# Optimization experiments

Hardware: AMD Instinct MI355X
Metric: run time of the kernel (lower is better)

The kernel has to match this reference:

```python
import jax, jax.numpy as jnp
import numpy as np

B, S, D, H = 4, 2048, 1024, 16
HD = D // H  # head_dim = 64


def setup_inputs() -> dict:
    key = jax.random.key(0)
    ks = jax.random.split(key, 9)
    sd = 1.0 / np.sqrt(D)
    x = jax.random.normal(ks[0], (B, S, D), dtype=jnp.float32)
    Wq = jax.random.normal(ks[1], (D, D), dtype=jnp.float32) * sd
    Wk = jax.random.normal(ks[2], (D, D), dtype=jnp.float32) * sd
    Wv = jax.random.normal(ks[3], (D, D), dtype=jnp.float32) * sd
    Wo = jax.random.normal(ks[4], (D, D), dtype=jnp.float32) * sd
    bq = jax.random.normal(ks[5], (D,), dtype=jnp.float32) * sd
    bk = jax.random.normal(ks[6], (D,), dtype=jnp.float32) * sd
    bv = jax.random.normal(ks[7], (D,), dtype=jnp.float32) * sd
    bo = jax.random.normal(ks[8], (D,), dtype=jnp.float32) * sd
    return {"x": x, "Wq": Wq, "bq": bq, "Wk": Wk, "bk": bk,
            "Wv": Wv, "bv": bv, "Wo": Wo, "bo": bo}


def reference(x, Wq, bq, Wk, bk, Wv, bv, Wo, bo):
    b, s, d = x.shape
    scale = jnp.float32(np.sqrt(HD))
    # projections, split into heads: (b, h, s, hd)
    def heads(y):
        return y.reshape(b, s, H, HD).transpose(0, 2, 1, 3)
    Q = heads(x @ Wq + bq)
    K = heads(x @ Wk + bk)
    V = heads(x @ Wv + bv)
    # (b, h, s, s) scores with causal mask
    scores = jnp.einsum('bhqd,bhkd->bhqk', Q, K) / scale
    causal = jnp.tril(jnp.ones((s, s), dtype=bool))
    scores = jnp.where(causal[None, None], scores, jnp.float32(-jnp.inf))
    probs = jax.nn.softmax(scores, axis=-1)
    out = jnp.einsum('bhqk,bhkd->bhqd', probs, V)
    out = out.transpose(0, 2, 1, 3).reshape(b, s, d)
    return out @ Wo + bo
```

## Files before the change

kernel.cpp:

```cpp
#include <hip/hip_runtime.h>
#include <hip/hip_bf16.h>
#include <cstdint>

typedef __bf16 bf16x8 __attribute__((ext_vector_type(8)));
typedef float f32x4 __attribute__((ext_vector_type(4)));
typedef float f32x16 __attribute__((ext_vector_type(16)));
typedef unsigned short u16t;

__device__ __forceinline__ u16t f2bf(float f) {
    uint32_t u = __builtin_bit_cast(uint32_t, f);
    u += 0x7FFF + ((u >> 16) & 1);
    return (u16t)(u >> 16);
}

constexpr int Bb = 4, Ss = 2048, Dd = 1024, Hh = 16;
constexpr int Mrows = Bb * Ss;
constexpr float NEG = -1e30f;
constexpr float QSCALE = 0.125f * 1.44269504088896340736f;

__global__ __launch_bounds__(256) void cvt_bf16(const float* __restrict__ in,
                                                u16t* __restrict__ out, int n) {
    int i = (blockIdx.x * 256 + threadIdx.x) * 4;
    if (i >= n) return;
    float4 v = *(const float4*)(in + i);
    u16t o[4] = {f2bf(v.x), f2bf(v.y), f2bf(v.z), f2bf(v.w)};
    *(ushort4*)(out + i) = *(ushort4*)o;
}

__global__ __launch_bounds__(256) void transpose_cvt4(const float* __restrict__ W0,
                                                      const float* __restrict__ W1,
                                                      const float* __restrict__ W2,
                                                      const float* __restrict__ W3,
                                                      u16t* __restrict__ Tqkv,
                                                      u16t* __restrict__ To) {
    __shared__ float tile[64][65];
    int z = blockIdx.z;
    const float* W = z == 0 ? W0 : z == 1 ? W1 : z == 2 ? W2 : W3;
    u16t* WT = z < 3 ? Tqkv + (size_t)z * Dd * Dd : To;
    int n0 = blockIdx.x * 64, k0 = blockIdx.y * 64;
    int c = threadIdx.x & 63, r0 = (threadIdx.x >> 6) * 16;
    for (int i = 0; i < 16; i++)
        tile[c][r0 + i] = W[(size_t)(k0 + r0 + i) * Dd + n0 + c];
    __syncthreads();
    for (int i = 0; i < 16; i++)
        WT[(size_t)(n0 + r0 + i) * Dd + k0 + c] = f2bf(tile[r0 + i][c]);
}

__global__ __launch_bounds__(256) void gemm_qkv(const u16t* __restrict__ A,
                                                const u16t* __restrict__ BT,
                                                const float* __restrict__ bq,
                                                const float* __restrict__ bk,
                                                const float* __restrict__ bvv,
                                                u16t* __restrict__ Qh,
                                                u16t* __restrict__ Kh,
                                                u16t* __restrict__ Vt) {
    __shared__ __align__(16) u16t Asm[128 * 32];
    __shared__ __align__(16) u16t Bsm[128 * 32];
    int tid = threadIdx.x, lane = tid & 63, w = tid >> 6;
    int wm = w >> 1, wn = w & 1;
    int ln = lane & 15, g = lane >> 4;
    int bid = blockIdx.x;
    int wg = (bid & 7) * 192 + (bid >> 3);
    int n0 = (wg % 24) * 128, m0 = (wg / 24) * 128;

    f32x4 acc[4][4] = {};

    int sr = w * 32 + (lane >> 2);
    int sc = (((lane & 3) ^ (sr & 3)) * 8);
    const u16t* Ag0 = A + (size_t)(m0 + sr) * Dd + sc;
    const u16t* Ag1 = A + (size_t)(m0 + sr + 16) * Dd + sc;
    const u16t* Bg0 = BT + (size_t)(n0 + sr) * Dd + sc;
    const u16t* Bg1 = BT + (size_t)(n0 + sr + 16) * Dd + sc;
    u16t* As0 = &Asm[(w * 32) * 32];
    u16t* As1 = &Asm[(w * 32 + 16) * 32];
    u16t* Bs0 = &Bsm[(w * 32) * 32];
    u16t* Bs1 = &Bsm[(w * 32 + 16) * 32];

    for (int k0 = 0; k0 < Dd; k0 += 32) {
        __syncthreads();
        __builtin_amdgcn_global_load_lds(Ag0 + k0, As0, 16, 0, 0);
        __builtin_amdgcn_global_load_lds(Ag1 + k0, As1, 16, 0, 0);
        __builtin_amdgcn_global_load_lds(Bg0 + k0, Bs0, 16, 0, 0);
        __builtin_amdgcn_global_load_lds(Bg1 + k0, Bs1, 16, 0, 0);
        __syncthreads();
        bf16x8 af[4], bf[4];
        #pragma unroll
        for (int i = 0; i < 4; i++) {
            int row = wm * 64 + i * 16 + ln;
            af[i] = *(const bf16x8*)&Asm[row * 32 + ((g ^ (row & 3)) * 8)];
        }
        #pragma unroll
        for (int j = 0; j < 4; j++) {
            int row = wn * 64 + j * 16 + ln;
            bf[j] = *(const bf16x8*)&Bsm[row * 32 + ((g ^ (row & 3)) * 8)];
        }
        #pragma unroll
        for (int i = 0; i < 4; i++)
            #pragma unroll
            for (int j = 0; j < 4; j++)
                acc[i][j] = __builtin_amdgcn_mfma_f32_16x16x32_bf16(af[i], bf[j], acc[i][j], 0, 0, 0);
    }

    #pragma unroll
    for (int i = 0; i < 4; i++) {
        #pragma unroll
        for (int j = 0; j < 4; j++) {
            int col = n0 + wn * 64 + j * 16 + ln;
            int seg = col >> 10, c1k = col & 1023;
            float bias = seg == 0 ? bq[c1k] : seg == 1 ? bk[c1k] : bvv[c1k];
            int rowb = m0 + wm * 64 + i * 16 + g * 4;
            int b = rowb >> 11, s = rowb & 2047, h = c1k >> 6, hd = c1k & 63;
            if (seg == 0) {
                for (int r = 0; r < 4; r++) {
                    float v = (acc[i][j][r] + bias) * QSCALE;
                    Qh[((size_t)(b * Hh + h) * Ss + s + r) * 64 + hd] = f2bf(v);
                }
            } else if (seg == 1) {
                for (int r = 0; r < 4; r++)
                    Kh[((size_t)(b * Hh + h) * Ss + s + r) * 64 + hd] = f2bf(acc[i][j][r] + bias);
            } else {
                u16t pk4[4];
                for (int r = 0; r < 4; r++) pk4[r] = f2bf(acc[i][j][r] + bias);
                *(ushort4*)(Vt + ((size_t)((b * Hh + h) * 64 + hd) << 11) + s) = *(ushort4*)pk4;
            }
        }
    }
}

__global__ __launch_bounds__(256) void gemm_o(const u16t* __restrict__ A,
                                              const u16t* __restrict__ BT,
                                              const float* __restrict__ bias,
                                              float* __restrict__ outF) {
    __shared__ __align__(16) u16t Asm[128 * 32];
    __shared__ __align__(16) u16t Bsm[128 * 32];
    int tid = threadIdx.x, lane = tid & 63, w = tid >> 6;
    int wm = w >> 1, wn = w & 1;
    int ln = lane & 15, g = lane >> 4;
    int bid = blockIdx.x;
    int wg = (bid & 7) * 64 + (bid >> 3);
    int n0 = (wg & 7) * 128, m0 = (wg >> 3) * 128;

    f32x4 acc[4][4] = {};

    int sr = w * 32 + (lane >> 2);
    int sc = (((lane & 3) ^ (sr & 3)) * 8);
    const u16t* Ag0 = A + (size_t)(m0 + sr) * Dd + sc;
    const u16t* Ag1 = A + (size_t)(m0 + sr + 16) * Dd + sc;
    const u16t* Bg0 = BT + (size_t)(n0 + sr) * Dd + sc;
    const u16t* Bg1 = BT + (size_t)(n0 + sr + 16) * Dd + sc;
    u16t* As0 = &Asm[(w * 32) * 32];
    u16t* As1 = &Asm[(w * 32 + 16) * 32];
    u16t* Bs0 = &Bsm[(w * 32) * 32];
    u16t* Bs1 = &Bsm[(w * 32 + 16) * 32];

    for (int k0 = 0; k0 < Dd; k0 += 32) {
        __syncthreads();
        __builtin_amdgcn_global_load_lds(Ag0 + k0, As0, 16, 0, 0);
        __builtin_amdgcn_global_load_lds(Ag1 + k0, As1, 16, 0, 0);
        __builtin_amdgcn_global_load_lds(Bg0 + k0, Bs0, 16, 0, 0);
        __builtin_amdgcn_global_load_lds(Bg1 + k0, Bs1, 16, 0, 0);
        __syncthreads();
        bf16x8 af[4], bf[4];
        #pragma unroll
        for (int i = 0; i < 4; i++) {
            int row = wm * 64 + i * 16 + ln;
            af[i] = *(const bf16x8*)&Asm[row * 32 + ((g ^ (row & 3)) * 8)];
        }
        #pragma unroll
        for (int j = 0; j < 4; j++) {
            int row = wn * 64 + j * 16 + ln;
            bf[j] = *(const bf16x8*)&Bsm[row * 32 + ((g ^ (row & 3)) * 8)];
        }
        #pragma unroll
        for (int i = 0; i < 4; i++)
            #pragma unroll
            for (int j = 0; j < 4; j++)
                acc[i][j] = __builtin_amdgcn_mfma_f32_16x16x32_bf16(af[i], bf[j], acc[i][j], 0, 0, 0);
    }

    #pragma unroll
    for (int i = 0; i < 4; i++) {
        #pragma unroll
        for (int j = 0; j < 4; j++) {
            int col = n0 + wn * 64 + j * 16 + ln;
            float bv = bias[col];
            int rowb = m0 + wm * 64 + i * 16 + g * 4;
            for (int r = 0; r < 4; r++)
                outF[(size_t)(rowb + r) * Dd + col] = acc[i][j][r] + bv;
        }
    }
}

__global__ __launch_bounds__(256) void attn(const u16t* __restrict__ Qh,
                                            const u16t* __restrict__ Kh,
                                            const u16t* __restrict__ Vt,
                                            u16t* __restrict__ Ob) {
    __shared__ __align__(16) u16t Ksm[2][64 * 64];
    __shared__ __align__(16) u16t Vsm[2][64 * 64];

    int tid = threadIdx.x, lane = tid & 63, w = tid >> 6;
    int l31 = lane & 31, hi = lane >> 5;
    int bh = blockIdx.y;

    const u16t* Kb = Kh + (size_t)bh * Ss * 64;
    const u16t* Vb = Vt + (size_t)bh * 64 * Ss;

    int sr0 = w * 16 + (lane >> 3);
    int sr1 = sr0 + 8;
    int sc0 = (((lane & 7) ^ (sr0 & 7) ^ ((sr0 >> 3) & 3)) * 8);
    int sc1 = (((lane & 7) ^ (sr1 & 7) ^ ((sr1 >> 3) & 3)) * 8);
    const u16t* Kg0 = Kb + (size_t)sr0 * 64 + sc0;
    const u16t* Kg1 = Kb + (size_t)sr1 * 64 + sc1;
    const u16t* Vg0 = Vb + (size_t)sr0 * Ss + sc0;
    const u16t* Vg1 = Vb + (size_t)sr1 * Ss + sc1;

    auto stage = [&](int buf, int t) {
        size_t koff = (size_t)t * 64 * 64;
        size_t voff = (size_t)t * 64;
        __builtin_amdgcn_global_load_lds(Kg0 + koff, &Ksm[buf][(w * 2 + 0) * 512], 16, 0, 0);
        __builtin_amdgcn_global_load_lds(Kg1 + koff, &Ksm[buf][(w * 2 + 1) * 512], 16, 0, 0);
        __builtin_amdgcn_global_load_lds(Vg0 + voff, &Vsm[buf][(w * 2 + 0) * 512], 16, 0, 0);
        __builtin_amdgcn_global_load_lds(Vg1 + voff, &Vsm[buf][(w * 2 + 1) * 512], 16, 0, 0);
    };

    int swzr = (l31 & 7) ^ ((l31 >> 3) & 3);

    for (int task = 0; task < 2; task++) {
        int qx = task == 0 ? (int)blockIdx.x : 15 - (int)blockIdx.x;
        int qb = qx * 128;
        int q0w = qb + w * 32;
        int qlane = q0w + l31;

        bf16x8 qB[4];
        {
            const u16t* Qp = Qh + ((size_t)bh * Ss + qlane) * 64 + hi * 8;
            #pragma unroll
            for (int ks = 0; ks < 4; ks++)
                qB[ks] = *(const bf16x8*)(Qp + 16 * ks);
        }

        f32x16 oacc[2] = {};
        float m_run = NEG, l_run = 0.f;
        int nt = (qb >> 6) + 2;

        stage(0, 0);
        __syncthreads();

        for (int t = 0; t < nt; t++) {
            int cur = t & 1;
            int kv0 = t << 6;
            if (t + 1 < nt) stage(cur ^ 1, t + 1);

            bool active = (kv0 <= q0w + 31);
            if (active) {
                f32x16 p0 = {}, p1 = {};
                __builtin_amdgcn_s_setprio(1);
                #pragma unroll
                for (int ks = 0; ks < 4; ks++) {
                    int cc = (2 * ks + hi) ^ swzr;
                    bf16x8 ka0 = *(const bf16x8*)&Ksm[cur][(size_t)l31 * 64 + cc * 8];
                    bf16x8 ka1 = *(const bf16x8*)&Ksm[cur][(size_t)(32 + l31) * 64 + cc * 8];
                    p0 = __builtin_amdgcn_mfma_f32_32x32x16_bf16(ka0, qB[ks], p0, 0, 0, 0);
                    p1 = __builtin_amdgcn_mfma_f32_32x32x16_bf16(ka1, qB[ks], p1, 0, 0, 0);
                }
                __builtin_amdgcn_s_setprio(0);

                float pv[32];
                #pragma unroll
                for (int r = 0; r < 16; r++) { pv[r] = p0[r]; pv[16 + r] = p1[r]; }

                if (kv0 + 63 > q0w) {
                    #pragma unroll
                    for (int ti = 0; ti < 2; ti++)
                        #pragma unroll
                        for (int r = 0; r < 16; r++) {
                            int kvg = kv0 + 32 * ti + (r & 3) + 8 * (r >> 2) + 4 * hi;
                            if (kvg > qlane) pv[16 * ti + r] = NEG;
                        }
                }

                float mt = fmaxf(pv[0], pv[1]);
                #pragma unroll
                for (int r = 2; r < 32; r += 2)
                    mt = fmaxf(fmaxf(mt, pv[r]), pv[r + 1]);
                mt = fmaxf(mt, __shfl_xor(mt, 32));
                if (__any(mt > m_run + 10.0f)) {
                    float mn = fmaxf(m_run, mt);
                    float al = __builtin_exp2f(m_run - mn);
                    m_run = mn;
                    l_run *= al;
                    #pragma unroll
                    for (int r = 0; r < 16; r++) { oacc[0][r] *= al; oacc[1][r] *= al; }
                }
                #pragma unroll
                for (int r = 0; r < 32; r++) pv[r] = __builtin_exp2f(pv[r] - m_run);
                float sa = 0.f, sb = 0.f, sc_ = 0.f, sd = 0.f;
                #pragma unroll
                for (int r = 0; r < 32; r += 4) {
                    sa += pv[r]; sb += pv[r + 1]; sc_ += pv[r + 2]; sd += pv[r + 3];
                }
                float rsum = (sa + sb) + (sc_ + sd);
                rsum += __shfl_xor(rsum, 32);
                l_run += rsum;

                bf16x8 pb[4];
                #pragma unroll
                for (int half = 0; half < 2; half++) {
                    const int base = 16 * half;
                    uint32_t c0, c1, c2, c3;
                    asm("v_cvt_pk_bf16_f32 %0, %1, %2" : "=v"(c0) : "v"(pv[base + 0]), "v"(pv[base + 1]));
                    asm("v_cvt_pk_bf16_f32 %0, %1, %2" : "=v"(c1) : "v"(pv[base + 2]), "v"(pv[base + 3]));
                    asm("v_cvt_pk_bf16_f32 %0, %1, %2" : "=v"(c2) : "v"(pv[base + 4]), "v"(pv[base + 5]));
                    asm("v_cvt_pk_bf16_f32 %0, %1, %2" : "=v"(c3) : "v"(pv[base + 6]), "v"(pv[base + 7]));
                    asm volatile("v_permlane32_swap_b32 %0, %1" : "+v"(c0), "+v"(c2));
                    asm volatile("v_permlane32_swap_b32 %0, %1" : "+v"(c1), "+v"(c3));
                    uint32_t w4[4] = {c0, c1, c2, c3};
                    pb[2 * half] = *(bf16x8*)w4;
                    uint32_t d0, d1, d2, d3;
                    asm("v_cvt_pk_bf16_f32 %0, %1, %2" : "=v"(d0) : "v"(pv[base + 8]),  "v"(pv[base + 9]));
                    asm("v_cvt_pk_bf16_f32 %0, %1, %2" : "=v"(d1) : "v"(pv[base + 10]), "v"(pv[base + 11]));
                    asm("v_cvt_pk_bf16_f32 %0, %1, %2" : "=v"(d2) : "v"(pv[base + 12]), "v"(pv[base + 13]));
                    asm("v_cvt_pk_bf16_f32 %0, %1, %2" : "=v"(d3) : "v"(pv[base + 14]), "v"(pv[base + 15]));
                    asm volatile("v_permlane32_swap_b32 %0, %1" : "+v"(d0), "+v"(d2));
                    asm volatile("v_permlane32_swap_b32 %0, %1" : "+v"(d1), "+v"(d3));
                    uint32_t w5[4] = {d0, d1, d2, d3};
                    pb[2 * half + 1] = *(bf16x8*)w5;
                }

                __builtin_amdgcn_s_setprio(1);
                #pragma unroll
                for (int dt = 0; dt < 2; dt++) {
                    int drow = dt * 32 + l31;
                    #pragma unroll
                    for (int ks = 0; ks < 4; ks++) {
                        int cc = (2 * ks + hi) ^ swzr;
                        bf16x8 va = *(const bf16x8*)&Vsm[cur][(size_t)drow * 64 + cc * 8];
                        oacc[dt] = __builtin_amdgcn_mfma_f32_32x32x16_bf16(va, pb[ks], oacc[dt], 0, 0, 0);
                    }
                }
                __builtin_amdgcn_s_setprio(0);
            }
            __syncthreads();
        }

        float inv = 1.0f / l_run;
        int b = bh >> 4, h = bh & 15;
        u16t* Op = Ob + ((size_t)(b * Ss + qlane)) * Dd + h * 64;
        #pragma unroll
        for (int dt = 0; dt < 2; dt++)
            #pragma unroll
            for (int rq = 0; rq < 4; rq++) {
                u16t pk4[4];
                #pragma unroll
                for (int j = 0; j < 4; j++) pk4[j] = f2bf(oacc[dt][rq * 4 + j] * inv);
                int d0 = dt * 32 + rq * 8 + hi * 4;
                *(ushort4*)(Op + d0) = *(ushort4*)pk4;
            }
    }
}

extern "C" void kernel_launch(void* const* d_in, const int* in_sizes, int n_in,
                              void* d_out, int out_size, void* d_ws, size_t ws_size,
                              hipStream_t stream) {
    const float* x  = (const float*)d_in[0];
    const float* Wq = (const float*)d_in[1];
    const float* bq = (const float*)d_in[2];
    const float* Wk = (const float*)d_in[3];
    const float* bk = (const float*)d_in[4];
    const float* Wv = (const float*)d_in[5];
    const float* bv = (const float*)d_in[6];
    const float* Wo = (const float*)d_in[7];
    const float* bo = (const float*)d_in[8];

    char* ws = (char*)d_ws;
    size_t off = 0;
    auto alloc = [&](size_t bytes) { char* p = ws + off; off += (bytes + 255) & ~(size_t)255; return p; };
    u16t* xb    = (u16t*)alloc((size_t)Mrows * Dd * 2);
    u16t* WqkvT = (u16t*)alloc((size_t)3 * Dd * Dd * 2);
    u16t* WoT   = (u16t*)alloc((size_t)Dd * Dd * 2);
    u16t* Qh    = (u16t*)alloc((size_t)Mrows * Dd * 2);
    u16t* Kh    = (u16t*)alloc((size_t)Mrows * Dd * 2);
    u16t* Vtp   = (u16t*)alloc((size_t)Mrows * Dd * 2);
    u16t* Ob    = (u16t*)alloc((size_t)Mrows * Dd * 2);

    int nx = Mrows * Dd;
    cvt_bf16<<<nx / (256 * 4), 256, 0, stream>>>(x, xb, nx);
    dim3 tg(16, 16, 4);
    transpose_cvt4<<<tg, 256, 0, stream>>>(Wq, Wk, Wv, Wo, WqkvT, WoT);

    gemm_qkv<<<1536, 256, 0, stream>>>(xb, WqkvT, bq, bk, bv, Qh, Kh, Vtp);

    dim3 ga(8, Bb * Hh);
    attn<<<ga, 256, 0, stream>>>(Qh, Kh, Vtp, Ob);

    gemm_o<<<512, 256, 0, stream>>>(Ob, WoT, bo, (float*)d_out);
}
```

Before: 206.0 us.

## Split causal attention KV range into two halves with separate merge kernel

Each attention block now computes two KV-range halves for different query tiles, one for tile i and one for tile 15-i. Each half writes an unnormalized bf16 partial output plus its running max and sum. A new merge kernel combines each pair of halves with log-sum-exp weights, which doubles the grid and balances work per block. The change also remaps blocks so each XCD works on the same heads, adds launch bounds for 4 blocks per CU, and reuses dead workspace buffers for the partials. It costs an extra kernel launch, extra global traffic for the partials, and a bf16 rounding step on the unnormalized partial outputs.

```diff
diff --git a/kernel.cpp b/kernel.cpp
--- a/kernel.cpp
+++ b/kernel.cpp
@@ -11,6 +11,10 @@
     uint32_t u = __builtin_bit_cast(uint32_t, f);
     u += 0x7FFF + ((u >> 16) & 1);
     return (u16t)(u >> 16);
+}
+__device__ __forceinline__ float bf2f(u16t v) {
+    uint32_t u = (uint32_t)v << 16;
+    return __builtin_bit_cast(float, u);
 }
 
 constexpr int Bb = 4, Ss = 2048, Dd = 1024, Hh = 16;
@@ -191,16 +195,20 @@
     }
 }
 
-__global__ __launch_bounds__(256) void attn(const u16t* __restrict__ Qh,
-                                            const u16t* __restrict__ Kh,
-                                            const u16t* __restrict__ Vt,
-                                            u16t* __restrict__ Ob) {
+__global__ __launch_bounds__(256, 4) void attn(const u16t* __restrict__ Qh,
+                                               const u16t* __restrict__ Kh,
+                                               const u16t* __restrict__ Vt,
+                                               u16t* __restrict__ Opart,
+                                               float2* __restrict__ ml) {
     __shared__ __align__(16) u16t Ksm[2][64 * 64];
     __shared__ __align__(16) u16t Vsm[2][64 * 64];
 
     int tid = threadIdx.x, lane = tid & 63, w = tid >> 6;
     int l31 = lane & 31, hi = lane >> 5;
-    int bh = blockIdx.y;
+    int flat = blockIdx.y * 16 + blockIdx.x;
+    int xcd = flat & 7, jj = flat >> 3;
+    int bh = xcd * 8 + (jj >> 4);
+    int i = jj & 15;
 
     const u16t* Kb = Kh + (size_t)bh * Ss * 64;
     const u16t* Vb = Vt + (size_t)bh * 64 * Ss;
@@ -226,7 +234,9 @@
     int swzr = (l31 & 7) ^ ((l31 >> 3) & 3);
 
     for (int task = 0; task < 2; task++) {
-        int qx = task == 0 ? (int)blockIdx.x : 15 - (int)blockIdx.x;
+        int qx = task == 0 ? i : 15 - i;
+        int tstart = task == 0 ? 0 : qx + 1;
+        int tend = task == 0 ? qx + 1 : 2 * qx + 2;
         int qb = qx * 128;
         int q0w = qb + w * 32;
         int qlane = q0w + l31;
@@ -241,15 +251,14 @@
 
         f32x16 oacc[2] = {};
         float m_run = NEG, l_run = 0.f;
-        int nt = (qb >> 6) + 2;
-
-        stage(0, 0);
+
+        stage(0, tstart);
         __syncthreads();
 
-        for (int t = 0; t < nt; t++) {
-            int cur = t & 1;
+        for (int t = tstart; t < tend; t++) {
+            int cur = (t - tstart) & 1;
             int kv0 = t << 6;
-            if (t + 1 < nt) stage(cur ^ 1, t + 1);
+            if (t + 1 < tend) stage(cur ^ 1, t + 1);
 
             bool active = (kv0 <= q0w + 31);
             if (active) {
@@ -343,19 +352,56 @@
             __syncthreads();
         }
 
-        float inv = 1.0f / l_run;
-        int b = bh >> 4, h = bh & 15;
-        u16t* Op = Ob + ((size_t)(b * Ss + qlane)) * Dd + h * 64;
+        int u = (bh * 16 + qx) * 2 + task;
+        int qloc = w * 32 + l31;
+        if (hi == 0) {
+            float2 v;
+            v.x = m_run; v.y = l_run;
+            ml[u * 128 + qloc] = v;
+        }
+        u16t* Op = Opart + ((size_t)u * 128 + qloc) * 64;
         #pragma unroll
         for (int dt = 0; dt < 2; dt++)
             #pragma unroll
             for (int rq = 0; rq < 4; rq++) {
                 u16t pk4[4];
                 #pragma unroll
-                for (int j = 0; j < 4; j++) pk4[j] = f2bf(oacc[dt][rq * 4 + j] * inv);
+                for (int j = 0; j < 4; j++) pk4[j] = f2bf(oacc[dt][rq * 4 + j]);
                 int d0 = dt * 32 + rq * 8 + hi * 4;
                 *(ushort4*)(Op + d0) = *(ushort4*)pk4;
             }
+    }
+}
+
+__global__ __launch_bounds__(256) void attn_merge(const u16t* __restrict__ Opart,
+                                                  const float2* __restrict__ ml,
+                                                  u16t* __restrict__ Ob) {
+    int r = blockIdx.x * 256 + threadIdx.x;
+    int bh = r >> 11, q = r & 2047;
+    int qx = q >> 7, qloc = q & 127;
+    int u0 = (bh * 16 + qx) * 2, u1 = u0 + 1;
+    float2 a = ml[u0 * 128 + qloc];
+    float2 b = ml[u1 * 128 + qloc];
+    float m = fmaxf(a.x, b.x);
+    float e0 = __builtin_exp2f(a.x - m);
+    float e1 = __builtin_exp2f(b.x - m);
+    float inv = 1.0f / (a.y * e0 + b.y * e1);
+    float f0 = e0 * inv, f1 = e1 * inv;
+    const uint4* p0 = (const uint4*)(Opart + ((size_t)u0 * 128 + qloc) * 64);
+    const uint4* p1 = (const uint4*)(Opart + ((size_t)u1 * 128 + qloc) * 64);
+    int bb = bh >> 4, hh = bh & 15;
+    u16t* dst = Ob + ((size_t)(bb * Ss + q)) * Dd + hh * 64;
+    #pragma unroll
+    for (int c = 0; c < 8; c++) {
+        uint4 x = p0[c], y = p1[c];
+        const u16t* px = (const u16t*)&x;
+        const u16t* py = (const u16t*)&y;
+        uint4 o;
+        u16t* po = (u16t*)&o;
+        #pragma unroll
+        for (int k = 0; k < 8; k++)
+            po[k] = f2bf(bf2f(px[k]) * f0 + bf2f(py[k]) * f1);
+        *(uint4*)(dst + c * 8) = o;
     }
 }
 
@@ -372,16 +418,21 @@
     const float* Wo = (const float*)d_in[7];
     const float* bo = (const float*)d_in[8];
 
+    constexpr size_t MB = 1024 * 1024;
     char* ws = (char*)d_ws;
     size_t off = 0;
     auto alloc = [&](size_t bytes) { char* p = ws + off; off += (bytes + 255) & ~(size_t)255; return p; };
-    u16t* xb    = (u16t*)alloc((size_t)Mrows * Dd * 2);
-    u16t* WqkvT = (u16t*)alloc((size_t)3 * Dd * Dd * 2);
-    u16t* WoT   = (u16t*)alloc((size_t)Dd * Dd * 2);
-    u16t* Qh    = (u16t*)alloc((size_t)Mrows * Dd * 2);
-    u16t* Kh    = (u16t*)alloc((size_t)Mrows * Dd * 2);
-    u16t* Vtp   = (u16t*)alloc((size_t)Mrows * Dd * 2);
-    u16t* Ob    = (u16t*)alloc((size_t)Mrows * Dd * 2);
+
+    char* R = alloc(34 * MB);
+    float2* ml   = (float2*)R;
+    u16t* Opart  = (u16t*)(R + 2 * MB);
+    u16t* xb     = (u16t*)R;
+    u16t* WqkvT  = (u16t*)(R + 16 * MB);
+    u16t* WoT    = (u16t*)alloc((size_t)Dd * Dd * 2);
+    u16t* Qh     = (u16t*)alloc((size_t)Mrows * Dd * 2);
+    u16t* Kh     = (u16t*)alloc((size_t)Mrows * Dd * 2);
+    u16t* Vtp    = (u16t*)alloc((size_t)Mrows * Dd * 2);
+    u16t* Ob     = Qh;
 
     int nx = Mrows * Dd;
     cvt_bf16<<<nx / (256 * 4), 256, 0, stream>>>(x, xb, nx);
@@ -390,8 +441,9 @@
 
     gemm_qkv<<<1536, 256, 0, stream>>>(xb, WqkvT, bq, bk, bv, Qh, Kh, Vtp);
 
-    dim3 ga(8, Bb * Hh);
-    attn<<<ga, 256, 0, stream>>>(Qh, Kh, Vtp, Ob);
+    dim3 ga(16, Bb * Hh);
+    attn<<<ga, 256, 0, stream>>>(Qh, Kh, Vtp, Opart, ml);
+    attn_merge<<<512, 256, 0, stream>>>(Opart, ml, Ob);
 
     gemm_o<<<512, 256, 0, stream>>>(Ob, WoT, bo, (float*)d_out);
 }
```

After: 219.2 us. +6.4%, slower.

## Process 128-key KV tiles per iteration and remap blocks by XCD

Applied to the files above, without the earlier changes.

The attention loop now stages 128 keys of K and V per iteration instead of 64. This halves the barrier and prefetch round-trips and amortises the softmax max/rescale over two sub-tiles, which are computed together with shared reductions. Block indices are remapped so that all q-tiles of a (batch, head) pair land on the same XCD, improving L2 reuse of K/V. The cost is double the LDS footprint (64 KB), higher register pressure from four score accumulators, and coarser causal skipping.

```diff
diff --git a/kernel.cpp b/kernel.cpp
--- a/kernel.cpp
+++ b/kernel.cpp
@@ -195,38 +195,56 @@
                                             const u16t* __restrict__ Kh,
                                             const u16t* __restrict__ Vt,
                                             u16t* __restrict__ Ob) {
-    __shared__ __align__(16) u16t Ksm[2][64 * 64];
-    __shared__ __align__(16) u16t Vsm[2][64 * 64];
+    __shared__ __align__(16) u16t Ksm[2][128 * 64];
+    __shared__ __align__(16) u16t Vsm[2][128 * 64];
 
     int tid = threadIdx.x, lane = tid & 63, w = tid >> 6;
     int l31 = lane & 31, hi = lane >> 5;
-    int bh = blockIdx.y;
+    int flat = blockIdx.y * 8 + blockIdx.x;
+    int xcd = flat & 7, jj = flat >> 3;
+    int bh = xcd * 8 + (jj >> 3);
+    int ip = jj & 7;
 
     const u16t* Kb = Kh + (size_t)bh * Ss * 64;
     const u16t* Vb = Vt + (size_t)bh * 64 * Ss;
 
-    int sr0 = w * 16 + (lane >> 3);
-    int sr1 = sr0 + 8;
-    int sc0 = (((lane & 7) ^ (sr0 & 7) ^ ((sr0 >> 3) & 3)) * 8);
-    int sc1 = (((lane & 7) ^ (sr1 & 7) ^ ((sr1 >> 3) & 3)) * 8);
-    const u16t* Kg0 = Kb + (size_t)sr0 * 64 + sc0;
-    const u16t* Kg1 = Kb + (size_t)sr1 * 64 + sc1;
-    const u16t* Vg0 = Vb + (size_t)sr0 * Ss + sc0;
-    const u16t* Vg1 = Vb + (size_t)sr1 * Ss + sc1;
-
-    auto stage = [&](int buf, int t) {
-        size_t koff = (size_t)t * 64 * 64;
-        size_t voff = (size_t)t * 64;
-        __builtin_amdgcn_global_load_lds(Kg0 + koff, &Ksm[buf][(w * 2 + 0) * 512], 16, 0, 0);
-        __builtin_amdgcn_global_load_lds(Kg1 + koff, &Ksm[buf][(w * 2 + 1) * 512], 16, 0, 0);
-        __builtin_amdgcn_global_load_lds(Vg0 + voff, &Vsm[buf][(w * 2 + 0) * 512], 16, 0, 0);
-        __builtin_amdgcn_global_load_lds(Vg1 + voff, &Vsm[buf][(w * 2 + 1) * 512], 16, 0, 0);
+    const u16t* KgP[4];
+    const u16t* VgP[4];
+    int ldsOff[4];
+    #pragma unroll
+    for (int i2 = 0; i2 < 4; i2++) {
+        int kr = w * 32 + i2 * 8 + (lane >> 3);
+        int kc = ((lane & 7) ^ (kr & 7) ^ ((kr >> 3) & 3)) * 8;
+        KgP[i2] = Kb + (size_t)kr * 64 + kc;
+        int vd = kr & 63, vcb = (kr >> 6) * 64;
+        VgP[i2] = Vb + (size_t)vd * Ss + vcb + kc;
+        ldsOff[i2] = (w * 32 + i2 * 8) * 64;
+    }
+    int swzr = (l31 & 7) ^ ((l31 >> 3) & 3);
+
+    auto pack2 = [&](const f32x16& p, bf16x8* out) {
+        uint32_t c0, c1, c2, c3;
+        asm("v_cvt_pk_bf16_f32 %0, %1, %2" : "=v"(c0) : "v"(p[0]), "v"(p[1]));
+        asm("v_cvt_pk_bf16_f32 %0, %1, %2" : "=v"(c1) : "v"(p[2]), "v"(p[3]));
+        asm("v_cvt_pk_bf16_f32 %0, %1, %2" : "=v"(c2) : "v"(p[4]), "v"(p[5]));
+        asm("v_cvt_pk_bf16_f32 %0, %1, %2" : "=v"(c3) : "v"(p[6]), "v"(p[7]));
+        asm volatile("v_permlane32_swap_b32 %0, %1" : "+v"(c0), "+v"(c2));
+        asm volatile("v_permlane32_swap_b32 %0, %1" : "+v"(c1), "+v"(c3));
+        uint32_t w4[4] = {c0, c1, c2, c3};
+        out[0] = *(bf16x8*)w4;
+        uint32_t d0, d1, d2, d3;
+        asm("v_cvt_pk_bf16_f32 %0, %1, %2" : "=v"(d0) : "v"(p[8]),  "v"(p[9]));
+        asm("v_cvt_pk_bf16_f32 %0, %1, %2" : "=v"(d1) : "v"(p[10]), "v"(p[11]));
+        asm("v_cvt_pk_bf16_f32 %0, %1, %2" : "=v"(d2) : "v"(p[12]), "v"(p[13]));
+        asm("v_cvt_pk_bf16_f32 %0, %1, %2" : "=v"(d3) : "v"(p[14]), "v"(p[15]));
+        asm volatile("v_permlane32_swap_b32 %0, %1" : "+v"(d0), "+v"(d2));
+        asm volatile("v_permlane32_swap_b32 %0, %1" : "+v"(d1), "+v"(d3));
+        uint32_t w5[4] = {d0, d1, d2, d3};
+        out[1] = *(bf16x8*)w5;
     };
 
-    int swzr = (l31 & 7) ^ ((l31 >> 3) & 3);
-
     for (int task = 0; task < 2; task++) {
-        int qx = task == 0 ? (int)blockIdx.x : 15 - (int)blockIdx.x;
+        int qx = task == 0 ? ip : 15 - ip;
         int qb = qx * 128;
         int q0w = qb + w * 32;
         int qlane = q0w + l31;
@@ -241,105 +259,158 @@
 
         f32x16 oacc[2] = {};
         float m_run = NEG, l_run = 0.f;
-        int nt = (qb >> 6) + 2;
-
-        stage(0, 0);
+        int npairs = qx + 1;
+
+        #pragma unroll
+        for (int i2 = 0; i2 < 4; i2++) {
+            __builtin_amdgcn_global_load_lds(KgP[i2], &Ksm[0][ldsOff[i2]], 16, 0, 0);
+            __builtin_amdgcn_global_load_lds(VgP[i2], &Vsm[0][ldsOff[i2]], 16, 0, 0);
+        }
         __syncthreads();
 
-        for (int t = 0; t < nt; t++) {
-            int cur = t & 1;
-            int kv0 = t << 6;
-            if (t + 1 < nt) stage(cur ^ 1, t + 1);
-
-            bool active = (kv0 <= q0w + 31);
-            if (active) {
-                f32x16 p0 = {}, p1 = {};
-                __builtin_amdgcn_s_setprio(1);
+        for (int u = 0; u < npairs; u++) {
+            int cur = u & 1;
+            if (u + 1 < npairs) {
+                #pragma unroll
+                for (int i2 = 0; i2 < 4; i2++) {
+                    __builtin_amdgcn_global_load_lds(KgP[i2] + (size_t)(u + 1) * 8192,
+                                                     &Ksm[cur ^ 1][ldsOff[i2]], 16, 0, 0);
+                    __builtin_amdgcn_global_load_lds(VgP[i2] + (size_t)(u + 1) * 128,
+                                                     &Vsm[cur ^ 1][ldsOff[i2]], 16, 0, 0);
+                }
+            }
+            int kv0 = u * 128;
+            bool bAct = (kv0 + 64) <= q0w + 31;
+
+            f32x16 pa0 = {}, pa1 = {}, pb0 = {}, pb1 = {};
+            __builtin_amdgcn_s_setprio(1);
+            #pragma unroll
+            for (int ks = 0; ks < 4; ks++) {
+                int cc = (2 * ks + hi) ^ swzr;
+                bf16x8 ka0 = *(const bf16x8*)&Ksm[cur][(size_t)l31 * 64 + cc * 8];
+                bf16x8 ka1 = *(const bf16x8*)&Ksm[cur][(size_t)(32 + l31) * 64 + cc * 8];
+                pa0 = __builtin_amdgcn_mfma_f32_32x32x16_bf16(ka0, qB[ks], pa0, 0, 0, 0);
+                pa1 = __builtin_amdgcn_mfma_f32_32x32x16_bf16(ka1, qB[ks], pa1, 0, 0, 0);
+            }
+            if (bAct) {
                 #pragma unroll
                 for (int ks = 0; ks < 4; ks++) {
                     int cc = (2 * ks + hi) ^ swzr;
-                    bf16x8 ka0 = *(const bf16x8*)&Ksm[cur][(size_t)l31 * 64 + cc * 8];
-                    bf16x8 ka1 = *(const bf16x8*)&Ksm[cur][(size_t)(32 + l31) * 64 + cc * 8];
-                    p0 = __builtin_amdgcn_mfma_f32_32x32x16_bf16(ka0, qB[ks], p0, 0, 0, 0);
-                    p1 = __builtin_amdgcn_mfma_f32_32x32x16_bf16(ka1, qB[ks], p1, 0, 0, 0);
-                }
-                __builtin_amdgcn_s_setprio(0);
-
-                float pv[32];
-                #pragma unroll
-                for (int r = 0; r < 16; r++) { pv[r] = p0[r]; pv[16 + r] = p1[r]; }
-
-                if (kv0 + 63 > q0w) {
+                    bf16x8 kb0 = *(const bf16x8*)&Ksm[cur][(size_t)(64 + l31) * 64 + cc * 8];
+                    bf16x8 kb1 = *(const bf16x8*)&Ksm[cur][(size_t)(96 + l31) * 64 + cc * 8];
+                    pb0 = __builtin_amdgcn_mfma_f32_32x32x16_bf16(kb0, qB[ks], pb0, 0, 0, 0);
+                    pb1 = __builtin_amdgcn_mfma_f32_32x32x16_bf16(kb1, qB[ks], pb1, 0, 0, 0);
+                }
+            }
+            __builtin_amdgcn_s_setprio(0);
+
+            if (u == qx) {
+                #pragma unroll
+                for (int r = 0; r < 16; r++) {
+                    int kvg = kv0 + (r & 3) + 8 * (r >> 2) + 4 * hi;
+                    if (kvg > qlane)      pa0[r] = NEG;
+                    if (kvg + 32 > qlane) pa1[r] = NEG;
+                }
+                if (bAct) {
                     #pragma unroll
-                    for (int ti = 0; ti < 2; ti++)
-                        #pragma unroll
-                        for (int r = 0; r < 16; r++) {
-                            int kvg = kv0 + 32 * ti + (r & 3) + 8 * (r >> 2) + 4 * hi;
-                            if (kvg > qlane) pv[16 * ti + r] = NEG;
-                        }
-                }
-
-                float mt = fmaxf(pv[0], pv[1]);
-                #pragma unroll
-                for (int r = 2; r < 32; r += 2)
-                    mt = fmaxf(fmaxf(mt, pv[r]), pv[r + 1]);
-                mt = fmaxf(mt, __shfl_xor(mt, 32));
-                if (__any(mt > m_run + 10.0f)) {
-                    float mn = fmaxf(m_run, mt);
-                    float al = __builtin_exp2f(m_run - mn);
-                    m_run = mn;
-                    l_run *= al;
-                    #pragma unroll
-                    for (int r = 0; r < 16; r++) { oacc[0][r] *= al; oacc[1][r] *= al; }
-                }
-                #pragma unroll
-                for (int r = 0; r < 32; r++) pv[r] = __builtin_exp2f(pv[r] - m_run);
-                float sa = 0.f, sb = 0.f, sc_ = 0.f, sd = 0.f;
-                #pragma unroll
-                for (int r = 0; r < 32; r += 4) {
-                    sa += pv[r]; sb += pv[r + 1]; sc_ += pv[r + 2]; sd += pv[r + 3];
-                }
-                float rsum = (sa + sb) + (sc_ + sd);
-                rsum += __shfl_xor(rsum, 32);
-                l_run += rsum;
-
-                bf16x8 pb[4];
-                #pragma unroll
-                for (int half = 0; half < 2; half++) {
-                    const int base = 16 * half;
-                    uint32_t c0, c1, c2, c3;
-                    asm("v_cvt_pk_bf16_f32 %0, %1, %2" : "=v"(c0) : "v"(pv[base + 0]), "v"(pv[base + 1]));
-                    asm("v_cvt_pk_bf16_f32 %0, %1, %2" : "=v"(c1) : "v"(pv[base + 2]), "v"(pv[base + 3]));
-                    asm("v_cvt_pk_bf16_f32 %0, %1, %2" : "=v"(c2) : "v"(pv[base + 4]), "v"(pv[base + 5]));
-                    asm("v_cvt_pk_bf16_f32 %0, %1, %2" : "=v"(c3) : "v"(pv[base + 6]), "v"(pv[base + 7]));
-                    asm volatile("v_permlane32_swap_b32 %0, %1" : "+v"(c0), "+v"(c2));
-                    asm volatile("v_permlane32_swap_b32 %0, %1" : "+v"(c1), "+v"(c3));
-                    uint32_t w4[4] = {c0, c1, c2, c3};
-                    pb[2 * half] = *(bf16x8*)w4;
-                    uint32_t d0, d1, d2, d3;
-                    asm("v_cvt_pk_bf16_f32 %0, %1, %2" : "=v"(d0) : "v"(pv[base + 8]),  "v"(pv[base + 9]));
-                    asm("v_cvt_pk_bf16_f32 %0, %1, %2" : "=v"(d1) : "v"(pv[base + 10]), "v"(pv[base + 11]));
-                    asm("v_cvt_pk_bf16_f32 %0, %1, %2" : "=v"(d2) : "v"(pv[base + 12]), "v"(pv[base + 13]));
-                    asm("v_cvt_pk_bf16_f32 %0, %1, %2" : "=v"(d3) : "v"(pv[base + 14]), "v"(pv[base + 15]));
-                    asm volatile("v_permlane32_swap_b32 %0, %1" : "+v"(d0), "+v"(d2));
-                    asm volatile("v_permlane32_swap_b32 %0, %1" : "+v"(d1), "+v"(d3));
-                    uint32_t w5[4] = {d0, d1, d2, d3};
-                    pb[2 * half + 1] = *(bf16x8*)w5;
-                }
-
-                __builtin_amdgcn_s_setprio(1);
+                    for (int r = 0; r < 16; r++) {
+                        int kvg = kv0 + (r & 3) + 8 * (r >> 2) + 4 * hi;
+                        if (kvg + 64 > qlane) pb0[r] = NEG;
+                        if (kvg + 96 > qlane) pb1[r] = NEG;
+                    }
+                }
+            }
+
+            float ma = fmaxf(pa0[0], pa1[0]), mb = fmaxf(pa0[1], pa1[1]);
+            float mc = fmaxf(pa0[2], pa1[2]), md = fmaxf(pa0[3], pa1[3]);
+            #pragma unroll
+            for (int r = 4; r < 16; r += 4) {
+                ma = fmaxf(ma, fmaxf(pa0[r], pa1[r]));
+                mb = fmaxf(mb, fmaxf(pa0[r + 1], pa1[r + 1]));
+                mc = fmaxf(mc, fmaxf(pa0[r + 2], pa1[r + 2]));
+                md = fmaxf(md, fmaxf(pa0[r + 3], pa1[r + 3]));
+            }
+            if (bAct) {
+                #pragma unroll
+                for (int r = 0; r < 16; r += 4) {
+                    ma = fmaxf(ma, fmaxf(pb0[r], pb1[r]));
+                    mb = fmaxf(mb, fmaxf(pb0[r + 1], pb1[r + 1]));
+                    mc = fmaxf(mc, fmaxf(pb0[r + 2], pb1[r + 2]));
+                    md = fmaxf(md, fmaxf(pb0[r + 3], pb1[r + 3]));
+                }
+            }
+            float mt = fmaxf(fmaxf(ma, mb), fmaxf(mc, md));
+            mt = fmaxf(mt, __shfl_xor(mt, 32));
+            if (__any(mt > m_run + 10.0f)) {
+                float mn = fmaxf(m_run, mt);
+                float al = __builtin_exp2f(m_run - mn);
+                m_run = mn;
+                l_run *= al;
+                #pragma unroll
+                for (int r = 0; r < 16; r++) { oacc[0][r] *= al; oacc[1][r] *= al; }
+            }
+            #pragma unroll
+            for (int r = 0; r < 16; r++) {
+                pa0[r] = __builtin_exp2f(pa0[r] - m_run);
+                pa1[r] = __builtin_exp2f(pa1[r] - m_run);
+            }
+            if (bAct) {
+                #pragma unroll
+                for (int r = 0; r < 16; r++) {
+                    pb0[r] = __builtin_exp2f(pb0[r] - m_run);
+                    pb1[r] = __builtin_exp2f(pb1[r] - m_run);
+                }
+            }
+            float sa = 0.f, sb = 0.f, sc2 = 0.f, sd = 0.f;
+            #pragma unroll
+            for (int r = 0; r < 16; r += 4) {
+                sa += pa0[r] + pa1[r];
+                sb += pa0[r + 1] + pa1[r + 1];
+                sc2 += pa0[r + 2] + pa1[r + 2];
+                sd += pa0[r + 3] + pa1[r + 3];
+            }
+            if (bAct) {
+                #pragma unroll
+                for (int r = 0; r < 16; r += 4) {
+                    sa += pb0[r] + pb1[r];
+                    sb += pb0[r + 1] + pb1[r + 1];
+                    sc2 += pb0[r + 2] + pb1[r + 2];
+                    sd += pb0[r + 3] + pb1[r + 3];
+                }
+            }
+            float rsum = (sa + sb) + (sc2 + sd);
+            rsum += __shfl_xor(rsum, 32);
+            l_run += rsum;
+
+            bf16x8 fa[4], fb[4];
+            pack2(pa0, &fa[0]);
+            pack2(pa1, &fa[2]);
+            if (bAct) { pack2(pb0, &fb[0]); pack2(pb1, &fb[2]); }
+
+            __builtin_amdgcn_s_setprio(1);
+            #pragma unroll
+            for (int dt = 0; dt < 2; dt++) {
+                int drow = dt * 32 + l31;
+                #pragma unroll
+                for (int ks = 0; ks < 4; ks++) {
+                    int cc = (2 * ks + hi) ^ swzr;
+                    bf16x8 va = *(const bf16x8*)&Vsm[cur][(size_t)drow * 64 + cc * 8];
+                    oacc[dt] = __builtin_amdgcn_mfma_f32_32x32x16_bf16(va, fa[ks], oacc[dt], 0, 0, 0);
+                }
+            }
+            if (bAct) {
                 #pragma unroll
                 for (int dt = 0; dt < 2; dt++) {
-                    int drow = dt * 32 + l31;
+                    int drow = 64 + dt * 32 + l31;
                     #pragma unroll
                     for (int ks = 0; ks < 4; ks++) {
                         int cc = (2 * ks + hi) ^ swzr;
                         bf16x8 va = *(const bf16x8*)&Vsm[cur][(size_t)drow * 64 + cc * 8];
-                        oacc[dt] = __builtin_amdgcn_mfma_f32_32x32x16_bf16(va, pb[ks], oacc[dt], 0, 0, 0);
+                        oacc[dt] = __builtin_amdgcn_mfma_f32_32x32x16_bf16(va, fb[ks], oacc[dt], 0, 0, 0);
                     }
                 }
-                __builtin_amdgcn_s_setprio(0);
-            }
+            }
+            __builtin_amdgcn_s_setprio(0);
             __syncthreads();
         }
 
```

Result: slower. 229.5 us (+11.4%).
